# Performance work log

Measured on AMD Instinct MI355X. Metric: run time of the kernel, lower is better.

The kernel has to match this reference:

```python
import jax, jax.numpy as jnp
import numpy as np

NUM_CLASSES = 4
IMG_SIZE = 640.0
NUM_ANCHORS = 3
EPS = 1e-07


def _giou(px, py, pw, ph, tx, ty, tw, th):
    # corners
    x1n, y1n, x1x, y1x = px - pw / 2, py - ph / 2, px + pw / 2, py + ph / 2
    x2n, y2n, x2x, y2x = tx - tw / 2, ty - th / 2, tx + tw / 2, ty + th / 2
    iw = jnp.clip(jnp.minimum(x1x, x2x) - jnp.maximum(x1n, x2n), 0.0)
    ih = jnp.clip(jnp.minimum(y1x, y2x) - jnp.maximum(y1n, y2n), 0.0)
    inter = iw * ih
    union = pw * ph + tw * th - inter + EPS
    iou = inter / union
    ew = jnp.maximum(x1x, x2x) - jnp.minimum(x1n, x2n)
    eh = jnp.maximum(y1x, y2x) - jnp.minimum(y1n, y2n)
    enclose = ew * eh + EPS
    return iou - (enclose - union) / enclose


def _scale_losses(pred, h, w, anc3, targets):
    # pred: [B, 27, h, w]; anc3: [3,2] (pixels); targets: [B,T,5]
    B = pred.shape[0]
    C = pred.shape[1] // NUM_ANCHORS
    p = pred.reshape(B, NUM_ANCHORS, C, h, w).transpose(0, 1, 3, 4, 2)  # [B,A,h,w,C]
    grid_x = (jnp.arange(w, dtype=p.dtype) / w)[None, None, None, :]
    grid_y = (jnp.arange(h, dtype=p.dtype) / h)[None, None, :, None]
    pred_x = jax.nn.sigmoid(p[..., 0]) + grid_x
    pred_y = jax.nn.sigmoid(p[..., 1]) + grid_y
    pred_w = jnp.exp(p[..., 2]) * (anc3[:, 0] / IMG_SIZE).reshape(1, -1, 1, 1)
    pred_h = jnp.exp(p[..., 3]) * (anc3[:, 1] / IMG_SIZE).reshape(1, -1, 1, 1)
    z_conf = p[..., 4]
    z_cls = p[..., 5:5 + NUM_CLASSES]

    cls_id = targets[..., 0].astype(jnp.int32)                      # [B,T]
    tx, ty, tw, th = (targets[..., i] for i in range(1, 5))
    valid = ((tx >= 0) & (tx <= 1) & (ty >= 0) & (ty <= 1) &
             (tw > 0) & (tw <= 1) & (th > 0) & (th <= 1))

    # anchor matching on (w,h) IoU, argmax keeps first max like the loop
    aw = anc3[:, 0] / IMG_SIZE                                      # [A]
    ah = anc3[:, 1] / IMG_SIZE
    inter = jnp.minimum(tw[..., None], aw) * jnp.minimum(th[..., None], ah)
    union = tw[..., None] * th[..., None] + aw * ah - inter
    best = jnp.argmax(inter / (union + EPS), axis=-1)               # [B,T]

    gxi = jnp.clip(jnp.floor(tx * w).astype(jnp.int32), 0, w - 1)
    gyi = jnp.clip(jnp.floor(ty * h).astype(jnp.int32), 0, h - 1)
    b_idx = jnp.arange(B)[:, None]

    px = pred_x[b_idx, best, gyi, gxi]
    py = pred_y[b_idx, best, gyi, gxi]
    pw_ = pred_w[b_idx, best, gyi, gxi]
    ph_ = pred_h[b_idx, best, gyi, gxi]
    zc = z_conf[b_idx, best, gyi, gxi]                              # conf logit [B,T]
    zcl = z_cls[b_idx, best, gyi, gxi]                              # cls logits [B,T,NC]

    giou = _giou(px, py, pw_, ph_, tx, ty, tw, th)
    mask = (valid & (cls_id < NUM_CLASSES)).astype(p.dtype)

    box = jnp.sum(mask * (1.0 - giou))
    onehot = jax.nn.one_hot(cls_id, NUM_CLASSES, dtype=p.dtype)
    # BCE(sigmoid(z), t) = softplus(z) - t*z, mean over classes
    cls_bce = jnp.mean(jax.nn.softplus(zcl) - onehot * zcl, axis=-1)
    cls = jnp.sum(mask * cls_bce)
    conf_t = jnp.clip(jax.lax.stop_gradient(giou), 0.0, 1.0)
    conf = jnp.sum(mask * (jax.nn.softplus(zc) - conf_t * zc))
    n = jnp.sum(valid.astype(p.dtype))
    return box, cls, conf, n


def _neg_conf(pred, h, w, neg_idx):
    # negative-sample conf BCE vs 0: softplus(logit); per-image mean, summed over B
    B = pred.shape[0]
    C = pred.shape[1] // NUM_ANCHORS
    zc = pred.reshape(B, NUM_ANCHORS, C, h, w)[:, :, 4].reshape(B, -1)  # [B, A*h*w]
    taken = jnp.take_along_axis(zc, neg_idx.astype(jnp.int32), axis=1)  # [B,500]
    per_b = jnp.mean(jax.nn.softplus(taken), axis=1)                    # [B]
    n_neg = B * neg_idx.shape[1]
    return 0.5 * jnp.sum(per_b) / n_neg


def yolo_loss(p3_out, p4_out, p5_out, targets, anchors,
              neg_idx_p3, neg_idx_p4, neg_idx_p5):
    scales = [(80, 80, p3_out, 0, neg_idx_p3),
              (40, 40, p4_out, 3, neg_idx_p4),
              (20, 20, p5_out, 6, neg_idx_p5)]
    box = cls = conf = n = jnp.float32(0.0)
    for h, w, pred, a0, _ in scales:
        b, c, cf, nn_ = _scale_losses(pred, h, w, anchors[a0:a0 + 3], targets)
        box, cls, conf, n = box + b, cls + c, conf + cf, n + nn_
    denom = jnp.maximum(n, 1.0)
    has = (n > 0).astype(box.dtype)
    box = jnp.where(n > 0, box / denom, box)
    cls = jnp.where(n > 0, cls / denom, cls)
    conf = jnp.where(n > 0, conf / denom, conf)
    for h, w, pred, a0, nidx in scales:
        conf = conf + _neg_conf(pred, h, w, nidx)
    total = box + cls + conf
    return total, box, cls, conf


def setup_inputs() -> dict:
    key = jax.random.key(0)
    k = jax.random.split(key, 10)
    B, T = 64, 50
    p3 = jax.random.normal(k[0], (B, 27, 80, 80), jnp.float32)
    p4 = jax.random.normal(k[1], (B, 27, 40, 40), jnp.float32)
    p5 = jax.random.normal(k[2], (B, 27, 20, 20), jnp.float32)
    cls = jax.random.randint(k[3], (B, T), 0, NUM_CLASSES).astype(jnp.float32)
    xy = jax.random.uniform(k[4], (B, T, 2), jnp.float32)
    wh = jax.random.uniform(k[5], (B, T, 2), jnp.float32, 0.02, 0.5)
    targets = jnp.concatenate([cls[..., None], xy, wh], axis=-1)
    anchors = jnp.array([[10, 13], [16, 30], [33, 23], [30, 61], [62, 45],
                         [59, 119], [116, 90], [156, 198], [373, 326]], jnp.float32)
    neg3 = jax.random.randint(k[6], (B, 500), 0, 3 * 80 * 80, jnp.int32)
    neg4 = jax.random.randint(k[7], (B, 500), 0, 3 * 40 * 40, jnp.int32)
    neg5 = jax.random.randint(k[8], (B, 500), 0, 3 * 20 * 20, jnp.int32)
    return {"p3_out": p3, "p4_out": p4, "p5_out": p5, "targets": targets,
            "anchors": anchors, "neg_idx_p3": neg3, "neg_idx_p4": neg4,
            "neg_idx_p5": neg5}


def reference(p3_out, p4_out, p5_out, targets, anchors,
              neg_idx_p3, neg_idx_p4, neg_idx_p5):
    return yolo_loss(p3_out, p4_out, p5_out, targets, anchors,
                     neg_idx_p3, neg_idx_p4, neg_idx_p5)
```

## Files before the change

kernel.cpp:

```cpp
#include <hip/hip_runtime.h>
#include <math.h>

#define NUM_CLASSES 4
#define EPS 1e-7f
#define B_ 64
#define T_ 50
#define NNEG 500
#define NA 38
#define NB 128

__device__ __forceinline__ float softplusf(float x) {
    return fmaxf(x, 0.0f) + log1pf(expf(-fabsf(x)));
}

__device__ __forceinline__ float block_reduce256(float v, float* sdata) {
    int t = threadIdx.x;
    sdata[t] = v;
    __syncthreads();
    for (int s = 128; s > 0; s >>= 1) {
        if (t < s) sdata[t] += sdata[t + s];
        __syncthreads();
    }
    float r = sdata[0];
    __syncthreads();
    return r;
}

__global__ void __launch_bounds__(256) yolo_main(
        const float* __restrict__ pr3, const float* __restrict__ pr4,
        const float* __restrict__ pr5, const float* __restrict__ targets,
        const float* __restrict__ anchors,
        const int* __restrict__ ng3, const int* __restrict__ ng4,
        const int* __restrict__ ng5, float* __restrict__ ws) {
    __shared__ float sred[256];

    if (blockIdx.x < NA) {
        float box = 0.f, cls = 0.f, conf = 0.f, nv = 0.f;
        int idx = blockIdx.x * 256 + threadIdx.x;
        if (idx < 3 * B_ * T_) {
            int s   = idx / (B_ * T_);
            int rem = idx - s * (B_ * T_);
            int b   = rem / T_;
            int t   = rem - b * T_;

            int hw = (s == 0) ? 80 : ((s == 1) ? 40 : 20);
            const float* pred = (s == 0) ? pr3 : ((s == 1) ? pr4 : pr5);
            int a0 = 3 * s;

            const float* tg = targets + (size_t)(b * T_ + t) * 5;
            float clsf = tg[0], tx = tg[1], ty = tg[2], tw = tg[3], th = tg[4];

            bool valid = (tx >= 0.f) && (tx <= 1.f) && (ty >= 0.f) && (ty <= 1.f) &&
                         (tw > 0.f)  && (tw <= 1.f) && (th > 0.f)  && (th <= 1.f);

            int best = 0; float bestv = -1.f, awb = 0.f, ahb = 0.f;
            #pragma unroll
            for (int a = 0; a < 3; ++a) {
                float aw = anchors[(a0 + a) * 2 + 0] / 640.0f;
                float ah = anchors[(a0 + a) * 2 + 1] / 640.0f;
                float inter = fminf(tw, aw) * fminf(th, ah);
                float uni   = tw * th + aw * ah - inter;
                float r     = inter / (uni + EPS);
                if (r > bestv) { bestv = r; best = a; awb = aw; ahb = ah; }
            }

            int w = hw, h = hw;
            int gxi = (int)floorf(tx * (float)w); gxi = min(max(gxi, 0), w - 1);
            int gyi = (int)floorf(ty * (float)h); gyi = min(max(gyi, 0), h - 1);

            size_t chs = (size_t)h * (size_t)w;
            const float* base = pred + ((size_t)(b * 27 + best * 9) * (size_t)h + (size_t)gyi) * (size_t)w + (size_t)gxi;
            float c0 = base[0 * chs], c1 = base[1 * chs], c2 = base[2 * chs];
            float c3 = base[3 * chs], zc = base[4 * chs];
            float z0 = base[5 * chs], z1 = base[6 * chs];
            float z2 = base[7 * chs], z3 = base[8 * chs];

            float px  = 1.f / (1.f + expf(-c0)) + (float)gxi / (float)w;
            float py  = 1.f / (1.f + expf(-c1)) + (float)gyi / (float)h;
            float pw_ = expf(c2) * awb;
            float ph_ = expf(c3) * ahb;

            float x1n = px - pw_ * 0.5f, x1x = px + pw_ * 0.5f;
            float y1n = py - ph_ * 0.5f, y1x = py + ph_ * 0.5f;
            float x2n = tx - tw * 0.5f,  x2x = tx + tw * 0.5f;
            float y2n = ty - th * 0.5f,  y2x = ty + th * 0.5f;
            float iw = fmaxf(fminf(x1x, x2x) - fmaxf(x1n, x2n), 0.f);
            float ih = fmaxf(fminf(y1x, y2x) - fmaxf(y1n, y2n), 0.f);
            float inter = iw * ih;
            float uni = pw_ * ph_ + tw * th - inter + EPS;
            float iou = inter / uni;
            float ew = fmaxf(x1x, x2x) - fminf(x1n, x2n);
            float eh = fmaxf(y1x, y2x) - fminf(y1n, y2n);
            float enclose = ew * eh + EPS;
            float giou = iou - (enclose - uni) / enclose;

            int cid = (int)clsf;
            float mask = (valid && (cid < NUM_CLASSES)) ? 1.f : 0.f;

            box = mask * (1.f - giou);

            float sbce = softplusf(z0) + softplusf(z1) + softplusf(z2) + softplusf(z3);
            float zsel = (cid == 0) ? z0 : (cid == 1) ? z1 : (cid == 2) ? z2 : (cid == 3) ? z3 : 0.f;
            cls = mask * 0.25f * (sbce - zsel);

            float conf_t = fminf(fmaxf(giou, 0.f), 1.f);
            conf = mask * (softplusf(zc) - conf_t * zc);

            nv = valid ? 1.f : 0.f;
        }
        float rb = block_reduce256(box,  sred);
        float rc = block_reduce256(cls,  sred);
        float rf = block_reduce256(conf, sred);
        float rn = block_reduce256(nv,   sred);
        if (threadIdx.x == 0) {
            float* w4 = ws + (size_t)blockIdx.x * 4;
            w4[0] = rb; w4[1] = rc; w4[2] = rf; w4[3] = rn;
        }
    } else {
        float acc = 0.f;
        const int total = 3 * B_ * NNEG;
        for (int i = (blockIdx.x - NA) * 256 + threadIdx.x; i < total; i += NB * 256) {
            int s   = i / (B_ * NNEG);
            int rem = i - s * (B_ * NNEG);
            int b   = rem / NNEG;
            int j   = rem - b * NNEG;

            int hw = (s == 0) ? 80 : ((s == 1) ? 40 : 20);
            int chs = hw * hw;
            const float* pred = (s == 0) ? pr3 : ((s == 1) ? pr4 : pr5);
            const int* nix = (s == 0) ? ng3 : ((s == 1) ? ng4 : ng5);

            int id = nix[b * NNEG + j];
            int a   = id / chs;
            int pos = id - a * chs;
            float z = pred[(size_t)(b * 27 + a * 9 + 4) * (size_t)chs + (size_t)pos];
            acc += softplusf(z);
        }
        float r = block_reduce256(acc, sred);
        if (threadIdx.x == 0) ws[NA * 4 + (blockIdx.x - NA)] = r;
    }
}

__global__ void __launch_bounds__(256) yolo_final(const float* __restrict__ ws,
                                                  float* __restrict__ out) {
    __shared__ float sb[256], sc[256], sf[256], sn[256], sg[256];
    int t = threadIdx.x;
    float b = 0.f, c = 0.f, f = 0.f, n = 0.f;
    if (t < NA) {
        b = ws[t * 4 + 0]; c = ws[t * 4 + 1];
        f = ws[t * 4 + 2]; n = ws[t * 4 + 3];
    }
    float g = (t < NB) ? ws[NA * 4 + t] : 0.f;
    sb[t] = b; sc[t] = c; sf[t] = f; sn[t] = n; sg[t] = g;
    __syncthreads();
    for (int s = 128; s > 0; s >>= 1) {
        if (t < s) {
            sb[t] += sb[t + s]; sc[t] += sc[t + s]; sf[t] += sf[t + s];
            sn[t] += sn[t + s]; sg[t] += sg[t + s];
        }
        __syncthreads();
    }
    if (t == 0) {
        float box = sb[0], cls = sc[0], conf = sf[0], nn = sn[0], negsum = sg[0];
        float denom = fmaxf(nn, 1.f);
        if (nn > 0.f) { box /= denom; cls /= denom; conf /= denom; }
        float neg = 0.5f * negsum / ((float)NNEG * (float)(B_ * NNEG));
        conf += neg;
        float total = box + cls + conf;
        out[0] = total; out[1] = box; out[2] = cls; out[3] = conf;
    }
}

extern "C" void kernel_launch(void* const* d_in, const int* in_sizes, int n_in,
                              void* d_out, int out_size, void* d_ws, size_t ws_size,
                              hipStream_t stream) {
    const float* p3      = (const float*)d_in[0];
    const float* p4      = (const float*)d_in[1];
    const float* p5      = (const float*)d_in[2];
    const float* targets = (const float*)d_in[3];
    const float* anchors = (const float*)d_in[4];
    const int*   ng3     = (const int*)d_in[5];
    const int*   ng4     = (const int*)d_in[6];
    const int*   ng5     = (const int*)d_in[7];

    float* ws  = (float*)d_ws;
    float* out = (float*)d_out;

    yolo_main<<<dim3(NA + NB), dim3(256), 0, stream>>>(
        p3, p4, p5, targets, anchors, ng3, ng4, ng5, ws);
    yolo_final<<<dim3(1), dim3(256), 0, stream>>>(ws, out);
}
```

Before: 14.13 us.

## Fuse final reduction into main kernel via flag-based last-stage gather

```diff
diff --git a/kernel.cpp b/kernel.cpp
--- a/kernel.cpp
+++ b/kernel.cpp
@@ -6,37 +6,32 @@
 #define B_ 64
 #define T_ 50
 #define NNEG 500
-#define NA 38
-#define NB 128
+#define NPOSB 38
+#define NNEGB 375
+#define NBLK (NPOSB + NNEGB)
+#define MAGIC 0x13579BDFu
+#define WSTRIDE 8
 
 __device__ __forceinline__ float softplusf(float x) {
     return fmaxf(x, 0.0f) + log1pf(expf(-fabsf(x)));
 }
 
-__device__ __forceinline__ float block_reduce256(float v, float* sdata) {
-    int t = threadIdx.x;
-    sdata[t] = v;
-    __syncthreads();
-    for (int s = 128; s > 0; s >>= 1) {
-        if (t < s) sdata[t] += sdata[t + s];
-        __syncthreads();
-    }
-    float r = sdata[0];
-    __syncthreads();
-    return r;
-}
-
-__global__ void __launch_bounds__(256) yolo_main(
+__global__ void __launch_bounds__(256) yolo_fused(
         const float* __restrict__ pr3, const float* __restrict__ pr4,
         const float* __restrict__ pr5, const float* __restrict__ targets,
         const float* __restrict__ anchors,
         const int* __restrict__ ng3, const int* __restrict__ ng4,
-        const int* __restrict__ ng5, float* __restrict__ ws) {
-    __shared__ float sred[256];
-
-    if (blockIdx.x < NA) {
-        float box = 0.f, cls = 0.f, conf = 0.f, nv = 0.f;
-        int idx = blockIdx.x * 256 + threadIdx.x;
+        const int* __restrict__ ng5, float* __restrict__ ws,
+        float* __restrict__ out) {
+    __shared__ float sred[5][256];
+
+    const int bid = blockIdx.x;
+    const int tid = threadIdx.x;
+
+    float v0 = 0.f, v1 = 0.f, v2 = 0.f, v3 = 0.f, v4 = 0.f;
+
+    if (bid < NPOSB) {
+        int idx = bid * 256 + tid;
         if (idx < 3 * B_ * T_) {
             int s   = idx / (B_ * T_);
             int rem = idx - s * (B_ * T_);
@@ -97,77 +92,97 @@
             int cid = (int)clsf;
             float mask = (valid && (cid < NUM_CLASSES)) ? 1.f : 0.f;
 
-            box = mask * (1.f - giou);
+            v0 = mask * (1.f - giou);
 
             float sbce = softplusf(z0) + softplusf(z1) + softplusf(z2) + softplusf(z3);
             float zsel = (cid == 0) ? z0 : (cid == 1) ? z1 : (cid == 2) ? z2 : (cid == 3) ? z3 : 0.f;
-            cls = mask * 0.25f * (sbce - zsel);
+            v1 = mask * 0.25f * (sbce - zsel);
 
             float conf_t = fminf(fmaxf(giou, 0.f), 1.f);
-            conf = mask * (softplusf(zc) - conf_t * zc);
-
-            nv = valid ? 1.f : 0.f;
-        }
-        float rb = block_reduce256(box,  sred);
-        float rc = block_reduce256(cls,  sred);
-        float rf = block_reduce256(conf, sred);
-        float rn = block_reduce256(nv,   sred);
-        if (threadIdx.x == 0) {
-            float* w4 = ws + (size_t)blockIdx.x * 4;
-            w4[0] = rb; w4[1] = rc; w4[2] = rf; w4[3] = rn;
+            v2 = mask * (softplusf(zc) - conf_t * zc);
+
+            v3 = valid ? 1.f : 0.f;
         }
     } else {
-        float acc = 0.f;
-        const int total = 3 * B_ * NNEG;
-        for (int i = (blockIdx.x - NA) * 256 + threadIdx.x; i < total; i += NB * 256) {
-            int s   = i / (B_ * NNEG);
-            int rem = i - s * (B_ * NNEG);
-            int b   = rem / NNEG;
-            int j   = rem - b * NNEG;
-
-            int hw = (s == 0) ? 80 : ((s == 1) ? 40 : 20);
-            int chs = hw * hw;
-            const float* pred = (s == 0) ? pr3 : ((s == 1) ? pr4 : pr5);
-            const int* nix = (s == 0) ? ng3 : ((s == 1) ? ng4 : ng5);
-
-            int id = nix[b * NNEG + j];
-            int a   = id / chs;
-            int pos = id - a * chs;
-            float z = pred[(size_t)(b * 27 + a * 9 + 4) * (size_t)chs + (size_t)pos];
-            acc += softplusf(z);
-        }
-        float r = block_reduce256(acc, sred);
-        if (threadIdx.x == 0) ws[NA * 4 + (blockIdx.x - NA)] = r;
-    }
-}
-
-__global__ void __launch_bounds__(256) yolo_final(const float* __restrict__ ws,
-                                                  float* __restrict__ out) {
-    __shared__ float sb[256], sc[256], sf[256], sn[256], sg[256];
-    int t = threadIdx.x;
-    float b = 0.f, c = 0.f, f = 0.f, n = 0.f;
-    if (t < NA) {
-        b = ws[t * 4 + 0]; c = ws[t * 4 + 1];
-        f = ws[t * 4 + 2]; n = ws[t * 4 + 3];
-    }
-    float g = (t < NB) ? ws[NA * 4 + t] : 0.f;
-    sb[t] = b; sc[t] = c; sf[t] = f; sn[t] = n; sg[t] = g;
+        int i = (bid - NPOSB) * 256 + tid;
+        int s   = i / (B_ * NNEG);
+        int rem = i - s * (B_ * NNEG);
+        int b   = rem / NNEG;
+        int j   = rem - b * NNEG;
+
+        int hw = (s == 0) ? 80 : ((s == 1) ? 40 : 20);
+        int chs = hw * hw;
+        const float* pred = (s == 0) ? pr3 : ((s == 1) ? pr4 : pr5);
+        const int* nix = (s == 0) ? ng3 : ((s == 1) ? ng4 : ng5);
+
+        int id = nix[b * NNEG + j];
+        int a   = id / chs;
+        int pos = id - a * chs;
+        float z = pred[(size_t)(b * 27 + a * 9 + 4) * (size_t)chs + (size_t)pos];
+        v4 = softplusf(z);
+    }
+
+    sred[0][tid] = v0; sred[1][tid] = v1; sred[2][tid] = v2;
+    sred[3][tid] = v3; sred[4][tid] = v4;
     __syncthreads();
     for (int s = 128; s > 0; s >>= 1) {
-        if (t < s) {
-            sb[t] += sb[t + s]; sc[t] += sc[t + s]; sf[t] += sf[t + s];
-            sn[t] += sn[t + s]; sg[t] += sg[t + s];
+        if (tid < s) {
+            sred[0][tid] += sred[0][tid + s];
+            sred[1][tid] += sred[1][tid + s];
+            sred[2][tid] += sred[2][tid + s];
+            sred[3][tid] += sred[3][tid + s];
+            sred[4][tid] += sred[4][tid + s];
         }
         __syncthreads();
     }
-    if (t == 0) {
-        float box = sb[0], cls = sc[0], conf = sf[0], nn = sn[0], negsum = sg[0];
+    if (tid == 0) {
+        float* slot = ws + (size_t)bid * WSTRIDE;
+        slot[0] = sred[0][0]; slot[1] = sred[1][0]; slot[2] = sred[2][0];
+        slot[3] = sred[3][0]; slot[4] = sred[4][0];
+        __hip_atomic_store((unsigned int*)(slot + 5), MAGIC,
+                           __ATOMIC_RELEASE, __HIP_MEMORY_SCOPE_AGENT);
+    }
+
+    if (bid != 0) return;
+
+    float a0 = 0.f, a1 = 0.f, a2 = 0.f, a3 = 0.f, a4 = 0.f;
+    #pragma unroll
+    for (int half = 0; half < 2; ++half) {
+        int i = tid + half * 256;
+        if (i < NBLK) {
+            unsigned int* flag = (unsigned int*)(ws + (size_t)i * WSTRIDE + 5);
+            while (__hip_atomic_load(flag, __ATOMIC_ACQUIRE,
+                                     __HIP_MEMORY_SCOPE_AGENT) != MAGIC) {
+                __builtin_amdgcn_s_sleep(1);
+            }
+            const float* slot = ws + (size_t)i * WSTRIDE;
+            a0 += slot[0]; a1 += slot[1]; a2 += slot[2];
+            a3 += slot[3]; a4 += slot[4];
+            *flag = 0u;
+        }
+    }
+    __syncthreads();
+    sred[0][tid] = a0; sred[1][tid] = a1; sred[2][tid] = a2;
+    sred[3][tid] = a3; sred[4][tid] = a4;
+    __syncthreads();
+    for (int s = 128; s > 0; s >>= 1) {
+        if (tid < s) {
+            sred[0][tid] += sred[0][tid + s];
+            sred[1][tid] += sred[1][tid + s];
+            sred[2][tid] += sred[2][tid + s];
+            sred[3][tid] += sred[3][tid + s];
+            sred[4][tid] += sred[4][tid + s];
+        }
+        __syncthreads();
+    }
+    if (tid == 0) {
+        float box = sred[0][0], cls = sred[1][0], conf = sred[2][0];
+        float nn = sred[3][0], negsum = sred[4][0];
         float denom = fmaxf(nn, 1.f);
         if (nn > 0.f) { box /= denom; cls /= denom; conf /= denom; }
         float neg = 0.5f * negsum / ((float)NNEG * (float)(B_ * NNEG));
         conf += neg;
-        float total = box + cls + conf;
-        out[0] = total; out[1] = box; out[2] = cls; out[3] = conf;
+        out[0] = box + cls + conf; out[1] = box; out[2] = cls; out[3] = conf;
     }
 }
 
@@ -183,10 +198,7 @@
     const int*   ng4     = (const int*)d_in[6];
     const int*   ng5     = (const int*)d_in[7];
 
-    float* ws  = (float*)d_ws;
-    float* out = (float*)d_out;
-
-    yolo_main<<<dim3(NA + NB), dim3(256), 0, stream>>>(
-        p3, p4, p5, targets, anchors, ng3, ng4, ng5, ws);
-    yolo_final<<<dim3(1), dim3(256), 0, stream>>>(ws, out);
+    yolo_fused<<<dim3(NBLK), dim3(256), 0, stream>>>(
+        p3, p4, p5, targets, anchors, ng3, ng4, ng5,
+        (float*)d_ws, (float*)d_out);
 }
```

Result: slower. 14.48 us (+2.5%).
